# Kernel tuning notes

Measured on AMD Instinct MI355X. Metric: run time of the kernel, lower is better.

The kernel has to match this reference:

```python
import jax, jax.numpy as jnp
import numpy as np

N_GENERA = 4096
N_RANKS = 6
N_GROUPS = 256  # distinct taxa per rank (fill_max for labels)


def setup_inputs() -> dict:
    key = jax.random.key(0)
    k1, k2 = jax.random.split(key)
    F_genus = jax.random.normal(k1, (1024, N_GENERA), dtype=jnp.float32)
    labels = jax.random.randint(k2, (N_RANKS, N_GENERA), 0, N_GROUPS, dtype=jnp.int32)
    return {"F_genus": F_genus, "labels": labels}


def reference(F_genus, labels):
    # Original computes F_genus @ W_rank where W_rank[i,j] = (label[i]==label[j]).
    # That is exactly: out[b, j] = sum_{i: label[i]==label[j]} F[b, i]
    # i.e. a segment-sum over genus indices followed by a gather back to genera.
    def per_rank(lab):
        # F_genus.T: [N, B]; segment-sum over genera grouped by this rank's label
        seg = jax.ops.segment_sum(F_genus.T, lab, num_segments=N_GROUPS)  # [G, B]
        return seg[lab]  # gather back: [N, B]

    ranks_out = jax.vmap(per_rank)(labels)          # [R, N, B]
    ranks_out = jnp.transpose(ranks_out, (2, 1, 0))  # [B, N, R]
    # concat the identity (genus-level) channel last, matching the original order
    return jnp.concatenate([ranks_out, F_genus[:, :, None]], axis=2)  # [B, N, R+1]
```

## Files before the change

kernel.cpp:

```cpp
#include <hip/hip_runtime.h>

#define N_GENERA 4096
#define N_RANKS 6
#define N_GROUPS 256
#define NCH 7
#define SEG_SZ (N_RANKS * N_GROUPS)
#define EXT_SZ (SEG_SZ + N_GENERA)
#define NF (N_GENERA * NCH)
#define NF4 (NF / 4)

typedef float f32x4 __attribute__((ext_vector_type(4)));

#define WS_IDX_OFF  0
#define WS_OFFS_OFF 98304
#define WS_SIDX_OFF 104704

__global__ __launch_bounds__(256) void prep_kernel(
    const int* __restrict__ labels,
    int* __restrict__ idx,
    int* __restrict__ offs,
    short* __restrict__ sidx)
{
    const int t = threadIdx.x;

    if (blockIdx.x < N_RANKS) {
        const int r = blockIdx.x;
        const int* __restrict__ lab = labels + r * N_GENERA;

        __shared__ int cnt[N_GROUPS];
        __shared__ int scan[N_GROUPS];
        __shared__ int cur[N_GROUPS];

        cnt[t] = 0;
        __syncthreads();
        for (int i = t; i < N_GENERA; i += 256)
            atomicAdd(&cnt[lab[i]], 1);
        __syncthreads();

        int v = cnt[t];
        scan[t] = v;
        __syncthreads();
        #pragma unroll
        for (int s = 1; s < 256; s <<= 1) {
            int add = (t >= s) ? scan[t - s] : 0;
            __syncthreads();
            scan[t] += add;
            __syncthreads();
        }
        int start = scan[t] - v;
        cur[t] = start;
        offs[r * 260 + t] = start;
        if (t == 0) offs[r * 260 + 256] = N_GENERA;
        __syncthreads();
        for (int i = t; i < N_GENERA; i += 256) {
            int p = atomicAdd(&cur[lab[i]], 1);
            idx[r * N_GENERA + p] = i;
        }
    } else {
        const int f = (blockIdx.x - N_RANKS) * 256 + t;
        const int j = f / NCH;
        const int ch = f - j * NCH;
        int v;
        if (ch < N_RANKS)
            v = ch * N_GROUPS + labels[ch * N_GENERA + j];
        else
            v = SEG_SZ + j;
        sidx[f] = (short)v;
    }
}

__global__ __launch_bounds__(512) void fused_kernel(
    const float* __restrict__ F,
    const int* __restrict__ idx,
    const int* __restrict__ offs,
    const short* __restrict__ sidx,
    float* __restrict__ out)
{
    __shared__ float2 ext2[EXT_SZ];
    const int b0 = blockIdx.x * 2;
    const int t = threadIdx.x;

    const float2 z2 = {0.f, 0.f};
    ext2[t] = z2; ext2[t + 512] = z2; ext2[t + 1024] = z2;

    const f32x4* Fv0 = reinterpret_cast<const f32x4*>(F + (size_t)b0 * N_GENERA);
    const f32x4* Fv1 = reinterpret_cast<const f32x4*>(F + (size_t)(b0 + 1) * N_GENERA);
    f32x4* Flv = reinterpret_cast<f32x4*>(ext2 + SEG_SZ);
    #pragma unroll
    for (int k = 0; k < 2; ++k) {
        const f32x4 a = __builtin_nontemporal_load(Fv0 + t + k * 512);
        const f32x4 c = __builtin_nontemporal_load(Fv1 + t + k * 512);
        f32x4 lo, hi;
        lo[0] = a[0]; lo[1] = c[0]; lo[2] = a[1]; lo[3] = c[1];
        hi[0] = a[2]; hi[1] = c[2]; hi[2] = a[3]; hi[3] = c[3];
        Flv[2 * (t + k * 512)]     = lo;
        Flv[2 * (t + k * 512) + 1] = hi;
    }
    __syncthreads();

    const float2* __restrict__ Fl2 = ext2 + SEG_SZ;
    #pragma unroll
    for (int w = 0; w < 3; ++w) {
        const int item = t + w * 512;
        const int r = item >> 8;
        const int g = item & 255;
        const int e = offs[r * 260 + g + 1];
        int k = offs[r * 260 + g];
        const int* __restrict__ ip = idx + r * N_GENERA;
        float sa = 0.f, sb = 0.f;
        for (; k + 4 <= e; k += 4) {
            int i0 = ip[k], i1 = ip[k + 1], i2 = ip[k + 2], i3 = ip[k + 3];
            float2 v0 = Fl2[i0], v1 = Fl2[i1], v2 = Fl2[i2], v3 = Fl2[i3];
            sa += (v0.x + v1.x) + (v2.x + v3.x);
            sb += (v0.y + v1.y) + (v2.y + v3.y);
        }
        for (; k < e; ++k) {
            float2 v = Fl2[ip[k]];
            sa += v.x; sb += v.y;
        }
        float2 sp; sp.x = sa; sp.y = sb;
        ext2[item] = sp;
    }
    __syncthreads();

    f32x4* __restrict__ op0 = reinterpret_cast<f32x4*>(out) + (size_t)b0 * NF4;
    f32x4* __restrict__ op1 = op0 + NF4;
    #pragma unroll
    for (int kk = 0; kk < 14; ++kk) {
        const int q = kk * 512 + t;
        short4 s4 = *reinterpret_cast<const short4*>(sidx + q * 4);
        float2 p0 = ext2[s4.x];
        float2 p1 = ext2[s4.y];
        float2 p2 = ext2[s4.z];
        float2 p3 = ext2[s4.w];
        f32x4 va, vb;
        va[0] = p0.x; va[1] = p1.x; va[2] = p2.x; va[3] = p3.x;
        vb[0] = p0.y; vb[1] = p1.y; vb[2] = p2.y; vb[3] = p3.y;
        __builtin_nontemporal_store(va, op0 + q);
        __builtin_nontemporal_store(vb, op1 + q);
    }
}

extern "C" void kernel_launch(void* const* d_in, const int* in_sizes, int n_in,
                              void* d_out, int out_size, void* d_ws, size_t ws_size,
                              hipStream_t stream) {
    const float* F      = (const float*)d_in[0];
    const int*   labels = (const int*)d_in[1];
    float*       out    = (float*)d_out;

    const int B = in_sizes[0] / N_GENERA;
    char* ws = (char*)d_ws;
    int*   idx  = (int*)(ws + WS_IDX_OFF);
    int*   offs = (int*)(ws + WS_OFFS_OFF);
    short* sidx = (short*)(ws + WS_SIDX_OFF);

    const int sidx_blocks = NF / 256;
    prep_kernel<<<dim3(N_RANKS + sidx_blocks), dim3(256), 0, stream>>>(labels, idx, offs, sidx);
    fused_kernel<<<dim3(B / 2), dim3(512), 0, stream>>>(F, idx, offs, sidx, out);
}
```

Measured before the change: 43.05 us.

## Split fused kernel into segment-sum and chunked gather kernels with load-balanced groups

Replaces the single fused kernel with two stages. A seg kernel computes segment sums for four batch rows per block, visiting groups in a permutation sorted by group size so that wavefront work is balanced, and writes them to workspace. A gather kernel then splits each batch quad across four blocks over genus chunks, giving many more blocks for the output write. The price is an extra global round trip for the segment sums, an extra launch, and more prep work. The old fused path is kept as a fallback when the workspace is too small.

```diff
diff --git a/kernel.cpp b/kernel.cpp
--- a/kernel.cpp
+++ b/kernel.cpp
@@ -9,17 +9,30 @@
 #define NF (N_GENERA * NCH)
 #define NF4 (NF / 4)
 
+#define GT 448
+#define JCH 1024
+#define NCHUNK 4
+#define GRP_PER_BLK 1792
+#define EXT4_SZ (SEG_SZ + JCH)
+
 typedef float f32x4 __attribute__((ext_vector_type(4)));
 
-#define WS_IDX_OFF  0
-#define WS_OFFS_OFF 98304
-#define WS_SIDX_OFF 104704
+#define WS_IDX_OFF   0
+#define WS_OFFS_OFF  98304
+#define WS_SIDXN_OFF 104704
+#define WS_SIDXO_OFF 162048
+#define WS_PERM_OFF  219392
+#define WS_SEG_OFF   225536
+
+__device__ __forceinline__ int imin(int a, int b) { return a < b ? a : b; }
 
 __global__ __launch_bounds__(256) void prep_kernel(
     const int* __restrict__ labels,
     int* __restrict__ idx,
     int* __restrict__ offs,
-    short* __restrict__ sidx)
+    short* __restrict__ sidxN,
+    short* __restrict__ sidxO,
+    int* __restrict__ perm)
 {
     const int t = threadIdx.x;
 
@@ -56,7 +69,7 @@
             int p = atomicAdd(&cur[lab[i]], 1);
             idx[r * N_GENERA + p] = i;
         }
-    } else {
+    } else if (blockIdx.x < N_RANKS + 112) {
         const int f = (blockIdx.x - N_RANKS) * 256 + t;
         const int j = f / NCH;
         const int ch = f - j * NCH;
@@ -64,8 +77,158 @@
         if (ch < N_RANKS)
             v = ch * N_GROUPS + labels[ch * N_GENERA + j];
         else
+            v = SEG_SZ + (j & (JCH - 1));
+        sidxN[f] = (short)v;
+    } else if (blockIdx.x < N_RANKS + 224) {
+        const int f = (blockIdx.x - N_RANKS - 112) * 256 + t;
+        const int j = f / NCH;
+        const int ch = f - j * NCH;
+        int v;
+        if (ch < N_RANKS)
+            v = ch * N_GROUPS + labels[ch * N_GENERA + j];
+        else
             v = SEG_SZ + j;
-        sidx[f] = (short)v;
+        sidxO[f] = (short)v;
+    } else {
+        __shared__ int cnt[SEG_SZ];
+        __shared__ int hist[64];
+        __shared__ int base[64];
+        __shared__ int cur[64];
+        for (int i = t; i < SEG_SZ; i += 256) cnt[i] = 0;
+        if (t < 64) { hist[t] = 0; cur[t] = 0; }
+        __syncthreads();
+        for (int r = 0; r < N_RANKS; ++r)
+            for (int i = t; i < N_GENERA; i += 256)
+                atomicAdd(&cnt[r * N_GROUPS + labels[r * N_GENERA + i]], 1);
+        __syncthreads();
+        for (int p = t; p < SEG_SZ; p += 256)
+            atomicAdd(&hist[imin(cnt[p], 63)], 1);
+        __syncthreads();
+        if (t < 64) {
+            int bsum = 0;
+            for (int c = t + 1; c < 64; ++c) bsum += hist[c];
+            base[t] = bsum;
+        }
+        __syncthreads();
+        for (int p = t; p < SEG_SZ; p += 256) {
+            int c = imin(cnt[p], 63);
+            int slot = base[c] + atomicAdd(&cur[c], 1);
+            perm[slot] = p;
+        }
+    }
+}
+
+__global__ __launch_bounds__(512) void seg_kernel(
+    const float* __restrict__ F,
+    const int* __restrict__ idx,
+    const int* __restrict__ offs,
+    const int* __restrict__ perm,
+    float* __restrict__ seg)
+{
+    __shared__ f32x4 F4[N_GENERA];
+    const int q = blockIdx.x;
+    const int b0 = q * 4;
+    const int t = threadIdx.x;
+
+    const f32x4* Fv0 = reinterpret_cast<const f32x4*>(F + (size_t)b0 * N_GENERA);
+    const f32x4* Fv1 = reinterpret_cast<const f32x4*>(F + (size_t)(b0 + 1) * N_GENERA);
+    const f32x4* Fv2 = reinterpret_cast<const f32x4*>(F + (size_t)(b0 + 2) * N_GENERA);
+    const f32x4* Fv3 = reinterpret_cast<const f32x4*>(F + (size_t)(b0 + 3) * N_GENERA);
+    #pragma unroll
+    for (int w = 0; w < 2; ++w) {
+        const int T = t + w * 512;
+        const f32x4 a0 = __builtin_nontemporal_load(Fv0 + T);
+        const f32x4 a1 = __builtin_nontemporal_load(Fv1 + T);
+        const f32x4 a2 = __builtin_nontemporal_load(Fv2 + T);
+        const f32x4 a3 = __builtin_nontemporal_load(Fv3 + T);
+        #pragma unroll
+        for (int k = 0; k < 4; ++k) {
+            f32x4 v;
+            v[0] = a0[k]; v[1] = a1[k]; v[2] = a2[k]; v[3] = a3[k];
+            F4[4 * T + k] = v;
+        }
+    }
+    __syncthreads();
+
+    f32x4* __restrict__ segq = reinterpret_cast<f32x4*>(seg) + (size_t)q * SEG_SZ;
+    #pragma unroll
+    for (int w = 0; w < 3; ++w) {
+        const int p = perm[w * 512 + t];
+        const int r = p >> 8;
+        const int g = p & 255;
+        const int e = offs[r * 260 + g + 1];
+        int k = offs[r * 260 + g];
+        const int* __restrict__ ip = idx + r * N_GENERA;
+        f32x4 s = {0.f, 0.f, 0.f, 0.f};
+        for (; k + 4 <= e; k += 4) {
+            const int i0 = ip[k], i1 = ip[k + 1], i2 = ip[k + 2], i3 = ip[k + 3];
+            f32x4 x0 = F4[i0], x1 = F4[i1], x2 = F4[i2], x3 = F4[i3];
+            s += (x0 + x1) + (x2 + x3);
+        }
+        for (; k < e; ++k) s += F4[ip[k]];
+        segq[p] = s;
+    }
+}
+
+__global__ __launch_bounds__(GT) void gather_kernel(
+    const float* __restrict__ F,
+    const float* __restrict__ seg,
+    const short* __restrict__ sidx,
+    float* __restrict__ out)
+{
+    __shared__ f32x4 ext4[EXT4_SZ];
+    const int blk = blockIdx.x;
+    const int q = blk >> 2;
+    const int c = blk & 3;
+    const int t = threadIdx.x;
+    const int b0 = q * 4;
+
+    const f32x4* sg = reinterpret_cast<const f32x4*>(seg) + (size_t)q * SEG_SZ;
+    for (int i = t; i < SEG_SZ; i += GT) ext4[i] = sg[i];
+
+    {
+        const int jbase = c * JCH;
+        const f32x4* Fq0 = reinterpret_cast<const f32x4*>(F + (size_t)b0 * N_GENERA + jbase);
+        const f32x4* Fq1 = reinterpret_cast<const f32x4*>(F + (size_t)(b0 + 1) * N_GENERA + jbase);
+        const f32x4* Fq2 = reinterpret_cast<const f32x4*>(F + (size_t)(b0 + 2) * N_GENERA + jbase);
+        const f32x4* Fq3 = reinterpret_cast<const f32x4*>(F + (size_t)(b0 + 3) * N_GENERA + jbase);
+        if (t < JCH / 4) {
+            const f32x4 a0 = __builtin_nontemporal_load(Fq0 + t);
+            const f32x4 a1 = __builtin_nontemporal_load(Fq1 + t);
+            const f32x4 a2 = __builtin_nontemporal_load(Fq2 + t);
+            const f32x4 a3 = __builtin_nontemporal_load(Fq3 + t);
+            #pragma unroll
+            for (int k = 0; k < 4; ++k) {
+                f32x4 v;
+                v[0] = a0[k]; v[1] = a1[k]; v[2] = a2[k]; v[3] = a3[k];
+                ext4[SEG_SZ + 4 * t + k] = v;
+            }
+        }
+    }
+    __syncthreads();
+
+    f32x4* __restrict__ op0 = reinterpret_cast<f32x4*>(out) + (size_t)b0 * NF4 + c * GRP_PER_BLK;
+    f32x4* __restrict__ op1 = op0 + NF4;
+    f32x4* __restrict__ op2 = op1 + NF4;
+    f32x4* __restrict__ op3 = op2 + NF4;
+    const short* __restrict__ sx = sidx + (size_t)c * (JCH * NCH);
+    #pragma unroll
+    for (int g = 0; g < 4; ++g) {
+        const int m = g * GT + t;
+        short4 s4 = *reinterpret_cast<const short4*>(sx + 4 * m);
+        f32x4 v0 = ext4[s4.x];
+        f32x4 v1 = ext4[s4.y];
+        f32x4 v2 = ext4[s4.z];
+        f32x4 v3 = ext4[s4.w];
+        f32x4 w0, w1, w2, w3;
+        w0[0] = v0[0]; w0[1] = v1[0]; w0[2] = v2[0]; w0[3] = v3[0];
+        w1[0] = v0[1]; w1[1] = v1[1]; w1[2] = v2[1]; w1[3] = v3[1];
+        w2[0] = v0[2]; w2[1] = v1[2]; w2[2] = v2[2]; w2[3] = v3[2];
+        w3[0] = v0[3]; w3[1] = v1[3]; w3[2] = v2[3]; w3[3] = v3[3];
+        __builtin_nontemporal_store(w0, op0 + m);
+        __builtin_nontemporal_store(w1, op1 + m);
+        __builtin_nontemporal_store(w2, op2 + m);
+        __builtin_nontemporal_store(w3, op3 + m);
     }
 }
 
@@ -127,8 +290,8 @@
     f32x4* __restrict__ op1 = op0 + NF4;
     #pragma unroll
     for (int kk = 0; kk < 14; ++kk) {
-        const int q = kk * 512 + t;
-        short4 s4 = *reinterpret_cast<const short4*>(sidx + q * 4);
+        const int qq = kk * 512 + t;
+        short4 s4 = *reinterpret_cast<const short4*>(sidx + qq * 4);
         float2 p0 = ext2[s4.x];
         float2 p1 = ext2[s4.y];
         float2 p2 = ext2[s4.z];
@@ -136,8 +299,8 @@
         f32x4 va, vb;
         va[0] = p0.x; va[1] = p1.x; va[2] = p2.x; va[3] = p3.x;
         vb[0] = p0.y; vb[1] = p1.y; vb[2] = p2.y; vb[3] = p3.y;
-        __builtin_nontemporal_store(va, op0 + q);
-        __builtin_nontemporal_store(vb, op1 + q);
+        __builtin_nontemporal_store(va, op0 + qq);
+        __builtin_nontemporal_store(vb, op1 + qq);
     }
 }
 
@@ -150,11 +313,22 @@
 
     const int B = in_sizes[0] / N_GENERA;
     char* ws = (char*)d_ws;
-    int*   idx  = (int*)(ws + WS_IDX_OFF);
-    int*   offs = (int*)(ws + WS_OFFS_OFF);
-    short* sidx = (short*)(ws + WS_SIDX_OFF);
-
-    const int sidx_blocks = NF / 256;
-    prep_kernel<<<dim3(N_RANKS + sidx_blocks), dim3(256), 0, stream>>>(labels, idx, offs, sidx);
-    fused_kernel<<<dim3(B / 2), dim3(512), 0, stream>>>(F, idx, offs, sidx, out);
-}
+    int*   idx   = (int*)(ws + WS_IDX_OFF);
+    int*   offs  = (int*)(ws + WS_OFFS_OFF);
+    short* sidxN = (short*)(ws + WS_SIDXN_OFF);
+    short* sidxO = (short*)(ws + WS_SIDXO_OFF);
+    int*   perm  = (int*)(ws + WS_PERM_OFF);
+    float* seg   = (float*)(ws + WS_SEG_OFF);
+
+    const size_t ws_need = (size_t)WS_SEG_OFF + (size_t)(B / 4) * SEG_SZ * 16;
+
+    prep_kernel<<<dim3(N_RANKS + 224 + 1), dim3(256), 0, stream>>>(
+        labels, idx, offs, sidxN, sidxO, perm);
+
+    if (ws_size >= ws_need && (B % 4) == 0) {
+        seg_kernel<<<dim3(B / 4), dim3(512), 0, stream>>>(F, idx, offs, perm, seg);
+        gather_kernel<<<dim3(B), dim3(GT), 0, stream>>>(F, seg, sidxN, out);
+    } else {
+        fused_kernel<<<dim3(B / 2), dim3(512), 0, stream>>>(F, idx, offs, sidxO, out);
+    }
+}
```

Result: slower. 77.47 us (+80.0%).

## Sort segments by length and transpose index lists for coalesced segment-sum

Applied to the files above, without the earlier changes.

Adds a prep block that counts every (rank, group) segment and orders segments by descending length, plus a second prep kernel that writes each segment's member indices in column-major (transposed) form. Neighbouring threads in a wavefront then handle segments of similar length, which cuts loop divergence, and their index loads become coalesced. Segments longer than a fixed cap fall back to the original index list. The cost is an extra kernel launch, more workspace traffic, and scattered shared-memory writes of the results by permuted segment id.

```diff
diff --git a/kernel.cpp b/kernel.cpp
--- a/kernel.cpp
+++ b/kernel.cpp
@@ -8,18 +8,26 @@
 #define EXT_SZ (SEG_SZ + N_GENERA)
 #define NF (N_GENERA * NCH)
 #define NF4 (NF / 4)
+#define MAXL 96
 
 typedef float f32x4 __attribute__((ext_vector_type(4)));
 
-#define WS_IDX_OFF  0
-#define WS_OFFS_OFF 98304
-#define WS_SIDX_OFF 104704
-
-__global__ __launch_bounds__(256) void prep_kernel(
+#define WS_IDX_OFF   0
+#define WS_OFFS_OFF  98304
+#define WS_SIDX_OFF  104704
+#define WS_PERM_OFF  162048
+#define WS_LENT_OFF  168192
+#define WS_IDXT_OFF  174336
+
+__device__ __forceinline__ int imin(int a, int b) { return a < b ? a : b; }
+
+__global__ __launch_bounds__(256) void prep1_kernel(
     const int* __restrict__ labels,
     int* __restrict__ idx,
     int* __restrict__ offs,
-    short* __restrict__ sidx)
+    short* __restrict__ sidx,
+    int* __restrict__ perm,
+    int* __restrict__ lenT)
 {
     const int t = threadIdx.x;
 
@@ -56,7 +64,7 @@
             int p = atomicAdd(&cur[lab[i]], 1);
             idx[r * N_GENERA + p] = i;
         }
-    } else {
+    } else if (blockIdx.x < N_RANKS + 112) {
         const int f = (blockIdx.x - N_RANKS) * 256 + t;
         const int j = f / NCH;
         const int ch = f - j * NCH;
@@ -66,22 +74,67 @@
         else
             v = SEG_SZ + j;
         sidx[f] = (short)v;
-    }
+    } else {
+        __shared__ int cnt[SEG_SZ];
+        __shared__ int hist[64];
+        __shared__ int base[64];
+        __shared__ int cur[64];
+        for (int i = t; i < SEG_SZ; i += 256) cnt[i] = 0;
+        if (t < 64) { hist[t] = 0; cur[t] = 0; }
+        __syncthreads();
+        for (int r = 0; r < N_RANKS; ++r)
+            for (int i = t; i < N_GENERA; i += 256)
+                atomicAdd(&cnt[r * N_GROUPS + labels[r * N_GENERA + i]], 1);
+        __syncthreads();
+        for (int p = t; p < SEG_SZ; p += 256)
+            atomicAdd(&hist[imin(cnt[p], 63)], 1);
+        __syncthreads();
+        if (t < 64) {
+            int bsum = 0;
+            for (int c = t + 1; c < 64; ++c) bsum += hist[c];
+            base[t] = bsum;
+        }
+        __syncthreads();
+        for (int p = t; p < SEG_SZ; p += 256) {
+            int c = imin(cnt[p], 63);
+            int slot = base[c] + atomicAdd(&cur[c], 1);
+            perm[slot] = p;
+            lenT[slot] = cnt[p];
+        }
+    }
+}
+
+__global__ __launch_bounds__(256) void prep2_kernel(
+    const int* __restrict__ idx,
+    const int* __restrict__ offs,
+    const int* __restrict__ perm,
+    int* __restrict__ idxT)
+{
+    const int s = blockIdx.x * 256 + threadIdx.x;
+    const int p = perm[s];
+    const int r = p >> 8;
+    const int g = p & 255;
+    const int beg = offs[r * 260 + g];
+    const int e   = offs[r * 260 + g + 1];
+    const int lm = imin(e - beg, MAXL);
+    const int* __restrict__ ip = idx + r * N_GENERA + beg;
+    for (int k = 0; k < lm; ++k)
+        idxT[k * SEG_SZ + s] = ip[k];
 }
 
 __global__ __launch_bounds__(512) void fused_kernel(
     const float* __restrict__ F,
     const int* __restrict__ idx,
     const int* __restrict__ offs,
+    const int* __restrict__ perm,
+    const int* __restrict__ lenT,
+    const int* __restrict__ idxT,
     const short* __restrict__ sidx,
     float* __restrict__ out)
 {
     __shared__ float2 ext2[EXT_SZ];
     const int b0 = blockIdx.x * 2;
     const int t = threadIdx.x;
-
-    const float2 z2 = {0.f, 0.f};
-    ext2[t] = z2; ext2[t + 512] = z2; ext2[t + 1024] = z2;
 
     const f32x4* Fv0 = reinterpret_cast<const f32x4*>(F + (size_t)b0 * N_GENERA);
     const f32x4* Fv1 = reinterpret_cast<const f32x4*>(F + (size_t)(b0 + 1) * N_GENERA);
@@ -101,25 +154,37 @@
     const float2* __restrict__ Fl2 = ext2 + SEG_SZ;
     #pragma unroll
     for (int w = 0; w < 3; ++w) {
-        const int item = t + w * 512;
-        const int r = item >> 8;
-        const int g = item & 255;
-        const int e = offs[r * 260 + g + 1];
-        int k = offs[r * 260 + g];
-        const int* __restrict__ ip = idx + r * N_GENERA;
+        const int s = t + w * 512;
+        const int p = perm[s];
+        const int len = lenT[s];
+        const int lm = imin(len, MAXL);
+        const int* __restrict__ col = idxT + s;
         float sa = 0.f, sb = 0.f;
-        for (; k + 4 <= e; k += 4) {
-            int i0 = ip[k], i1 = ip[k + 1], i2 = ip[k + 2], i3 = ip[k + 3];
+        int k = 0;
+        for (; k + 4 <= lm; k += 4) {
+            const int i0 = col[(k    ) * SEG_SZ];
+            const int i1 = col[(k + 1) * SEG_SZ];
+            const int i2 = col[(k + 2) * SEG_SZ];
+            const int i3 = col[(k + 3) * SEG_SZ];
             float2 v0 = Fl2[i0], v1 = Fl2[i1], v2 = Fl2[i2], v3 = Fl2[i3];
             sa += (v0.x + v1.x) + (v2.x + v3.x);
             sb += (v0.y + v1.y) + (v2.y + v3.y);
         }
-        for (; k < e; ++k) {
-            float2 v = Fl2[ip[k]];
+        for (; k < lm; ++k) {
+            float2 v = Fl2[col[k * SEG_SZ]];
             sa += v.x; sb += v.y;
         }
+        if (len > MAXL) {
+            const int r = p >> 8, g = p & 255;
+            const int beg = offs[r * 260 + g];
+            const int* __restrict__ ip = idx + r * N_GENERA + beg;
+            for (int k2 = MAXL; k2 < len; ++k2) {
+                float2 v = Fl2[ip[k2]];
+                sa += v.x; sb += v.y;
+            }
+        }
         float2 sp; sp.x = sa; sp.y = sb;
-        ext2[item] = sp;
+        ext2[p] = sp;
     }
     __syncthreads();
 
@@ -153,8 +218,13 @@
     int*   idx  = (int*)(ws + WS_IDX_OFF);
     int*   offs = (int*)(ws + WS_OFFS_OFF);
     short* sidx = (short*)(ws + WS_SIDX_OFF);
-
-    const int sidx_blocks = NF / 256;
-    prep_kernel<<<dim3(N_RANKS + sidx_blocks), dim3(256), 0, stream>>>(labels, idx, offs, sidx);
-    fused_kernel<<<dim3(B / 2), dim3(512), 0, stream>>>(F, idx, offs, sidx, out);
-}
+    int*   perm = (int*)(ws + WS_PERM_OFF);
+    int*   lenT = (int*)(ws + WS_LENT_OFF);
+    int*   idxT = (int*)(ws + WS_IDXT_OFF);
+
+    prep1_kernel<<<dim3(N_RANKS + 112 + 1), dim3(256), 0, stream>>>(
+        labels, idx, offs, sidx, perm, lenT);
+    prep2_kernel<<<dim3(SEG_SZ / 256), dim3(256), 0, stream>>>(idx, offs, perm, idxT);
+    fused_kernel<<<dim3(B / 2), dim3(512), 0, stream>>>(
+        F, idx, offs, perm, lenT, idxT, sidx, out);
+}
```

Measured after the change: 56.85 us. 1.32x slower.
